# Optimization experiments

Measured on AMD Instinct MI355X. Metric: run time of the kernel, lower is better.

## Reference

```python
import jax, jax.numpy as jnp
import numpy as np

C = 32        # channels
B = 4         # batch
H = W = 256   # spatial
K = 3         # adaptive kernel size
BN_EPS = 1e-5


def conv2d(x, w, b, pad):
    # x: [B,Cin,H,W], w: [Cout,Cin,kh,kw]
    y = jax.lax.conv_general_dilated(
        x, w, window_strides=(1, 1), padding=[(pad, pad), (pad, pad)],
        dimension_numbers=('NCHW', 'OIHW', 'NCHW'))
    return y + b[None, :, None, None]


def bn(x, g, beta, mu, var):
    scale = (g / jnp.sqrt(var + BN_EPS))[None, :, None, None]
    return (x - mu[None, :, None, None]) * scale + beta[None, :, None, None]


def res_block(x, w, b, g, beta, mu, var):
    # w: [2,C,C,3,3]; conv-BN-ReLU-conv-BN, residual add, ReLU
    h = bn(conv2d(x, w[0], b[0], 1), g[0], beta[0], mu[0], var[0])
    h = jax.nn.relu(h)
    h = bn(conv2d(h, w[1], b[1], 1), g[1], beta[1], mu[1], var[1])
    return jax.nn.relu(x + h)


def kernel_pred(frames, core, rate):
    # frames: [B,N,H,W] (color=1 squeezed), core: [B,N,K*K,H,W]
    b, n, h, w = frames.shape
    p = (K // 2) * rate
    fp = jnp.pad(frames, ((0, 0), (0, 0), (p, p), (p, p)))
    # stack K*K shifted copies along new axis 2 (same order as torch loop)
    stack = jnp.stack([fp[:, :, i * rate:i * rate + h, j * rate:j * rate + w]
                       for i in range(K) for j in range(K)], axis=2)
    return jnp.sum(core * stack, axis=2)  # [B,N,H,W]; white_level=1.0


def setup_inputs() -> dict:
    key = jax.random.key(0)
    ks = jax.random.split(key, 16)
    inp = {}
    inp['input'] = jax.random.normal(ks[0], (B, C, H, W), dtype=jnp.float32)
    # 4 residual blocks x 2 convs each
    inp['wconv'] = 0.05 * jax.random.normal(ks[1], (4, 2, C, C, 3, 3), dtype=jnp.float32)
    inp['bconv'] = jnp.zeros((4, 2, C), dtype=jnp.float32)
    inp['bn_gamma'] = jnp.ones((4, 2, C), dtype=jnp.float32) + 0.01 * jax.random.normal(ks[2], (4, 2, C), dtype=jnp.float32)
    inp['bn_beta'] = 0.01 * jax.random.normal(ks[3], (4, 2, C), dtype=jnp.float32)
    inp['bn_mean'] = 0.1 * jax.random.normal(ks[4], (4, 2, C), dtype=jnp.float32)
    inp['bn_var'] = 0.5 + jax.random.uniform(ks[5], (4, 2, C), dtype=jnp.float32)
    inp['tau'] = 0.5 * jnp.ones((1, C, 1, 1), dtype=jnp.float32)
    inp['w_outc'] = 0.05 * jax.random.normal(ks[6], (C * 9, C, 1, 1), dtype=jnp.float32)
    inp['b_outc'] = jnp.zeros((C * 9,), dtype=jnp.float32)
    inp['w_final'] = 0.05 * jax.random.normal(ks[7], (C, C * 4, 3, 3), dtype=jnp.float32)
    inp['b_final'] = jnp.zeros((C,), dtype=jnp.float32)
    return inp


def reference(input, wconv, bconv, bn_gamma, bn_beta, bn_mean, bn_var, tau,
              w_outc, b_outc, w_final, b_final):
    m = input
    for i in range(4):  # fixed small structural loop over residual blocks
        m = res_block(m, wconv[i], bconv[i], bn_gamma[i], bn_beta[i],
                      bn_mean[i], bn_var[i])
    m5 = jax.nn.relu(m - tau)
    core = conv2d(m5, w_outc, b_outc, 0)                    # [B, C*9, H, W]
    core = core.reshape(B, C, K * K, H, W)                  # [B, N, 9, H, W]
    preds = [kernel_pred(input, core, r) for r in (1, 2, 3, 4)]
    pred_cat = jnp.concatenate(preds, axis=1)               # [B, 4C, H, W]
    return conv2d(pred_cat, w_final, b_final, 1)            # [B, C, H, W]
```

## Files before the change

kernel.cpp:

```cpp
#include <hip/hip_runtime.h>

typedef __bf16 bf16;
typedef __attribute__((ext_vector_type(8))) __bf16 bf16x8;
typedef __attribute__((ext_vector_type(4))) float f32x4;

#define HH 256
#define WW 256
#define BB 4
#define NPIX 65536
#define AS 264
#define APX 69696
#define PS 258
#define PPX 66564

#define GLOAD16(SRC, DST) __builtin_amdgcn_global_load_lds( \
    (const __attribute__((address_space(1))) void*)(SRC),   \
    (__attribute__((address_space(3))) void*)(DST), 16, 0, 0)

__device__ inline bf16x8 bzero8() {
    bf16x8 v;
    #pragma unroll
    for (int i = 0; i < 8; ++i) v[i] = (bf16)0.0f;
    return v;
}

__device__ inline int chof(int s) {
    return 4 * (s >> 3) + 16 * ((s >> 2) & 1) + (s & 3);
}

__global__ __launch_bounds__(256) void prep_in(const float* __restrict__ in,
                                               bf16* __restrict__ outP) {
    int p = blockIdx.x * 256 + threadIdx.x;
    int b = p >> 16, rem = p & 65535;
    int y = rem >> 8, x = rem & 255;
    float ch[32];
    #pragma unroll
    for (int c = 0; c < 32; ++c)
        ch[c] = in[(size_t)(b * 32 + c) * NPIX + rem];
    bf16* o = outP + ((size_t)b * APX + (size_t)(y + 4) * AS + x + 4) * 32;
    #pragma unroll
    for (int g = 0; g < 4; ++g) {
        bf16x8 w;
        #pragma unroll
        for (int j = 0; j < 4; ++j) {
            w[j]     = (bf16)ch[4 * g + j];
            w[4 + j] = (bf16)ch[16 + 4 * g + j];
        }
        *reinterpret_cast<bf16x8*>(o + g * 8) = w;
    }
}

__global__ __launch_bounds__(256) void zero_halo(bf16* __restrict__ in0b,
                                                 bf16* __restrict__ actA,
                                                 bf16* __restrict__ actB,
                                                 bf16* __restrict__ pred) {
    int i = blockIdx.x * 256 + threadIdx.x;
    const int NA = 3 * 4 * 4160;
    if (i < NA) {
        int buf = i / (4 * 4160), r = i % (4 * 4160);
        int b = r / 4160, k = r % 4160;
        int y, x;
        if (k < 2112) { int rr = k / 264; y = rr < 4 ? rr : 256 + rr; x = k % 264; }
        else { int j = k - 2112; y = 4 + j / 8; int c8 = j % 8; x = c8 < 4 ? c8 : 256 + c8; }
        bf16* p = (buf == 0 ? in0b : buf == 1 ? actA : actB) +
                  ((size_t)b * APX + (size_t)y * AS + x) * 32;
        #pragma unroll
        for (int cg = 0; cg < 4; ++cg)
            *reinterpret_cast<bf16x8*>(p + cg * 8) = bzero8();
    } else if (i < NA + 4 * 1028) {
        int r = i - NA;
        int b = r / 1028, k = r % 1028;
        int y, x;
        if (k < 516) { int rr = k / 258; y = rr ? 257 : 0; x = k % 258; }
        else { int j = k - 516; y = 1 + j / 2; x = (j & 1) ? 257 : 0; }
        bf16* p = pred + ((size_t)b * PPX + (size_t)y * PS + x) * 128;
        #pragma unroll
        for (int cg = 0; cg < 16; ++cg)
            *reinterpret_cast<bf16x8*>(p + cg * 8) = bzero8();
    }
}

__global__ void fold_w(const float* __restrict__ wconv, const float* __restrict__ bconv,
                       const float* __restrict__ g, const float* __restrict__ beta,
                       const float* __restrict__ mu, const float* __restrict__ var,
                       const float* __restrict__ w_outc, const float* __restrict__ b_outc,
                       const float* __restrict__ w_final, const float* __restrict__ tau,
                       bf16* __restrict__ Wres, float* __restrict__ Bres,
                       bf16* __restrict__ Wcore, bf16* __restrict__ Wfin,
                       float* __restrict__ bCore, float* __restrict__ tauP) {
    int idx = blockIdx.x * 256 + threadIdx.x;
    if (idx < 73728) {
        int l = idx / 9216, r = idx % 9216;
        int tap = r >> 10, co = (r >> 5) & 31, ci = chof(r & 31);
        float s = g[l * 32 + co] * rsqrtf(var[l * 32 + co] + 1e-5f);
        Wres[idx] = (bf16)(wconv[l * 9216 + (co * 32 + ci) * 9 + tap] * s);
    } else if (idx < 73984) {
        int i = idx - 73728;
        float s = g[i] * rsqrtf(var[i] + 1e-5f);
        Bres[i] = (bconv[i] - mu[i]) * s + beta[i];
    } else if (idx < 83200) {
        int r = idx - 73984;
        int tap = r >> 10, nn = (r >> 5) & 31, ci = chof(r & 31);
        Wcore[r] = (bf16)w_outc[(nn * 9 + tap) * 32 + ci];
    } else if (idx < 120064) {
        int r = idx - 83200;
        int chunk = r / 9216, r2 = r % 9216;
        int tap = r2 >> 10, co = (r2 >> 5) & 31, n = chof(r2 & 31);
        Wfin[r] = (bf16)w_final[(size_t)(co * 128 + chunk * 32 + n) * 9 + tap];
    } else if (idx < 120352) {
        int r = idx - 120064;
        int tap = r >> 5, n = r & 31;
        bCore[r] = b_outc[n * 9 + tap];
    } else if (idx < 120384) {
        int s = idx - 120352;
        tauP[s] = tau[chof(s)];
    }
}

__global__ __launch_bounds__(256) void resblock_g(
    const bf16* __restrict__ in, const bf16* __restrict__ W1,
    const bf16* __restrict__ W2, const float* __restrict__ B1,
    const float* __restrict__ B2, bf16* __restrict__ out) {
    extern __shared__ char smem[];
    bf16* xs = (bf16*)smem;
    bf16* hs = (bf16*)(smem + 34816);
    const int x0 = blockIdx.x * 64, y0 = blockIdx.y * 4, b = blockIdx.z;
    const int tid = threadIdx.x;
    const int lane = tid & 63, wv = tid >> 6;
    const int col = lane & 15, g = lane >> 4;
    const bf16* inb = in + (size_t)b * APX * 32;

    for (int gi = wv; gi < 34; gi += 4) {
        int i = gi * 64 + lane;
        int px = i >> 2, s = i & 3;
        int yy = px / 68, xx = px % 68;
        int gsl = s ^ ((px >> 1) & 3);
        const bf16* src = inb + ((size_t)(y0 + yy + 2) * AS + x0 + xx + 2) * 32 + gsl * 8;
        GLOAD16(src, smem + gi * 1024);
    }

    bf16x8 Wf[9][2];
    #pragma unroll
    for (int tap = 0; tap < 9; ++tap) {
        Wf[tap][0] = *reinterpret_cast<const bf16x8*>(W1 + tap * 1024 + col * 32 + g * 8);
        Wf[tap][1] = *reinterpret_cast<const bf16x8*>(W1 + tap * 1024 + (16 + col) * 32 + g * 8);
    }
    f32x4 bb0 = *reinterpret_cast<const f32x4*>(B1 + 4 * g);
    f32x4 bb1 = *reinterpret_cast<const f32x4*>(B1 + 16 + 4 * g);
    __syncthreads();

    for (int u = wv; u < 30; u += 4) {
        int r = u / 5, s = u - 5 * r;
        int off = s * 16; if (off > 50) off = 50;
        const int hy = y0 + r - 1;
        const int hx = x0 + off + col - 1;
        f32x4 c0 = bb0, c1 = bb1;
        #pragma unroll
        for (int tap = 0; tap < 9; ++tap) {
            const int dy = tap / 3, dx = tap % 3;
            const int px = (r + dy) * 68 + off + col + dx;
            bf16x8 Bf = *reinterpret_cast<const bf16x8*>(
                xs + px * 32 + (g ^ ((px >> 1) & 3)) * 8);
            c0 = __builtin_amdgcn_mfma_f32_16x16x32_bf16(Wf[tap][0], Bf, c0, 0, 0, 0);
            c1 = __builtin_amdgcn_mfma_f32_16x16x32_bf16(Wf[tap][1], Bf, c1, 0, 0, 0);
        }
        bf16x8 o;
        #pragma unroll
        for (int j = 0; j < 4; ++j) {
            o[j]     = (bf16)fmaxf(c0[j], 0.0f);
            o[4 + j] = (bf16)fmaxf(c1[j], 0.0f);
        }
        if ((unsigned)hy >= HH || (unsigned)hx >= WW) o = bzero8();
        *reinterpret_cast<bf16x8*>(hs + (r * 66 + off + col) * 40 + g * 8) = o;
    }

    #pragma unroll
    for (int tap = 0; tap < 9; ++tap) {
        Wf[tap][0] = *reinterpret_cast<const bf16x8*>(W2 + tap * 1024 + col * 32 + g * 8);
        Wf[tap][1] = *reinterpret_cast<const bf16x8*>(W2 + tap * 1024 + (16 + col) * 32 + g * 8);
    }
    bb0 = *reinterpret_cast<const f32x4*>(B2 + 4 * g);
    bb1 = *reinterpret_cast<const f32x4*>(B2 + 16 + 4 * g);
    __syncthreads();

    bf16* outb = out + (size_t)b * APX * 32;
    const int y = y0 + wv;
    #pragma unroll
    for (int sg = 0; sg < 4; ++sg) {
        f32x4 c0 = bb0, c1 = bb1;
        #pragma unroll
        for (int tap = 0; tap < 9; ++tap) {
            const int dy = tap / 3, dx = tap % 3;
            bf16x8 Bf = *reinterpret_cast<const bf16x8*>(
                hs + ((wv + dy) * 66 + sg * 16 + col + dx) * 40 + g * 8);
            c0 = __builtin_amdgcn_mfma_f32_16x16x32_bf16(Wf[tap][0], Bf, c0, 0, 0, 0);
            c1 = __builtin_amdgcn_mfma_f32_16x16x32_bf16(Wf[tap][1], Bf, c1, 0, 0, 0);
        }
        const int pxr = (wv + 2) * 68 + sg * 16 + col + 2;
        bf16x8 xr = *reinterpret_cast<const bf16x8*>(
            xs + pxr * 32 + (g ^ ((pxr >> 1) & 3)) * 8);
        bf16x8 o;
        #pragma unroll
        for (int j = 0; j < 4; ++j) {
            o[j]     = (bf16)fmaxf(c0[j] + (float)xr[j], 0.0f);
            o[4 + j] = (bf16)fmaxf(c1[j] + (float)xr[4 + j], 0.0f);
        }
        *reinterpret_cast<bf16x8*>(
            outb + ((size_t)(y + 4) * AS + x0 + sg * 16 + col + 4) * 32 + g * 8) = o;
    }
}

__global__ __launch_bounds__(256) void final_conv_v5(
    const bf16* __restrict__ pred, const bf16* __restrict__ Wfin,
    const float* __restrict__ bfin, float* __restrict__ out) {
    __shared__ bf16 pt[2][12800];
    const int x0 = blockIdx.x * 64, y0 = blockIdx.y * 4, b = blockIdx.z;
    const int tid = threadIdx.x;
    const int lane = tid & 63, wv = tid >> 6;
    const int col = lane & 15, g = lane >> 4;
    const bf16* pb = pred + (size_t)b * PPX * 128;

    auto stage = [&](int c, int bi) {
        for (int gi = wv; gi < 25; gi += 4) {
            int i = gi * 64 + lane;
            int px = i >> 2; if (px > 395) px = 395;
            int s = i & 3;
            int yy = px / 66, xx = px % 66;
            int gsl = s ^ ((px >> 1) & 3);
            const bf16* src = pb + ((size_t)(y0 + yy) * PS + x0 + xx) * 128 + c * 32 + gsl * 8;
            GLOAD16(src, (char*)&pt[bi][0] + gi * 1024);
        }
    };

    f32x4 a0[4], a1[4];
    {
        f32x4 b0 = *reinterpret_cast<const f32x4*>(bfin + 4 * g);
        f32x4 b1 = *reinterpret_cast<const f32x4*>(bfin + 16 + 4 * g);
        #pragma unroll
        for (int i = 0; i < 4; ++i) { a0[i] = b0; a1[i] = b1; }
    }

    stage(0, 0);
    __syncthreads();

    for (int chunk = 0; chunk < 4; ++chunk) {
        const int cur = chunk & 1;
        bf16x8 Wf[9][2];
        #pragma unroll
        for (int tap = 0; tap < 9; ++tap) {
            Wf[tap][0] = *reinterpret_cast<const bf16x8*>(
                Wfin + chunk * 9216 + tap * 1024 + col * 32 + g * 8);
            Wf[tap][1] = *reinterpret_cast<const bf16x8*>(
                Wfin + chunk * 9216 + tap * 1024 + (16 + col) * 32 + g * 8);
        }
        if (chunk < 3) stage(chunk + 1, cur ^ 1);

        #pragma unroll
        for (int sg = 0; sg < 4; ++sg) {
            #pragma unroll
            for (int tap = 0; tap < 9; ++tap) {
                const int dy = tap / 3, dx = tap % 3;
                const int px = (wv + dy) * 66 + sg * 16 + col + dx;
                bf16x8 Bf = *reinterpret_cast<const bf16x8*>(
                    &pt[cur][0] + px * 32 + (g ^ ((px >> 1) & 3)) * 8);
                a0[sg] = __builtin_amdgcn_mfma_f32_16x16x32_bf16(Wf[tap][0], Bf, a0[sg], 0, 0, 0);
                a1[sg] = __builtin_amdgcn_mfma_f32_16x16x32_bf16(Wf[tap][1], Bf, a1[sg], 0, 0, 0);
            }
        }
        __syncthreads();
    }

    const int y = y0 + wv;
    #pragma unroll
    for (int sg = 0; sg < 4; ++sg) {
        const int x = x0 + sg * 16 + col;
        #pragma unroll
        for (int j = 0; j < 4; ++j) {
            out[(size_t)(b * 32 + 4 * g + j) * NPIX + (size_t)y * WW + x] = a0[sg][j];
            out[(size_t)(b * 32 + 16 + 4 * g + j) * NPIX + (size_t)y * WW + x] = a1[sg][j];
        }
    }
}

__global__ __launch_bounds__(256, 2) void core_pred_v4(
    const bf16* __restrict__ m, const bf16* __restrict__ framesP,
    const float* __restrict__ tauP, const bf16* __restrict__ WcoreG,
    const float* __restrict__ bCore, bf16* __restrict__ pred) {
    __shared__ bf16 fr[576 * 32];
    __shared__ bf16 Wc[9 * 32 * 32];
    const int x0 = blockIdx.x * 16, y0 = blockIdx.y * 16, b = blockIdx.z;
    const int tid = threadIdx.x;
    const int lane = tid & 63, wv = tid >> 6;
    const int col = lane & 15, g = lane >> 4;

    for (int i = tid; i < 1152; i += 256)
        *reinterpret_cast<bf16x8*>(Wc + i * 8) =
            *reinterpret_cast<const bf16x8*>(WcoreG + i * 8);
    const bf16* fb = framesP + (size_t)b * APX * 32;
    for (int i = tid; i < 2304; i += 256) {
        int px = i >> 2, cg = i & 3;
        int yy = px / 24, xx = px % 24;
        bf16x8 v = *reinterpret_cast<const bf16x8*>(
            fb + ((size_t)(y0 + yy) * AS + x0 + xx) * 32 + cg * 8);
        *reinterpret_cast<bf16x8*>(fr + px * 32 + cg * 8) = v;
    }
    float t8[8];
    #pragma unroll
    for (int k = 0; k < 8; ++k) t8[k] = tauP[g * 8 + k];
    __syncthreads();

    const bf16* mb = m + (size_t)b * APX * 32;
    bf16* pb = pred + (size_t)b * PPX * 128;

    #pragma unroll 1
    for (int uu = 0; uu < 4; ++uu) {
        const int yl = wv * 4 + uu;
        const int y = y0 + yl;

        bf16x8 Bv = *reinterpret_cast<const bf16x8*>(
            mb + ((size_t)(y + 4) * AS + x0 + col + 4) * 32 + g * 8);
        #pragma unroll
        for (int k = 0; k < 8; ++k)
            Bv[k] = (bf16)fmaxf((float)Bv[k] - t8[k], 0.0f);

        float acc[4][8];
        #pragma unroll
        for (int r = 0; r < 4; ++r)
            #pragma unroll
            for (int k = 0; k < 8; ++k) acc[r][k] = 0.0f;

        #pragma unroll
        for (int dy = 0; dy < 3; ++dy) {
            float core[3][8];
            #pragma unroll
            for (int dx = 0; dx < 3; ++dx) {
                const int tap = dy * 3 + dx;
                bf16x8 A0 = *reinterpret_cast<const bf16x8*>(
                    Wc + tap * 1024 + col * 32 + g * 8);
                bf16x8 A1 = *reinterpret_cast<const bf16x8*>(
                    Wc + tap * 1024 + (16 + col) * 32 + g * 8);
                f32x4 c0 = *reinterpret_cast<const f32x4*>(bCore + tap * 32 + 4 * g);
                f32x4 c1 = *reinterpret_cast<const f32x4*>(bCore + tap * 32 + 16 + 4 * g);
                c0 = __builtin_amdgcn_mfma_f32_16x16x32_bf16(A0, Bv, c0, 0, 0, 0);
                c1 = __builtin_amdgcn_mfma_f32_16x16x32_bf16(A1, Bv, c1, 0, 0, 0);
                #pragma unroll
                for (int j = 0; j < 4; ++j) {
                    core[dx][j]     = c0[j];
                    core[dx][4 + j] = c1[j];
                }
            }
            #pragma unroll
            for (int r = 1; r <= 4; ++r) {
                const int row = yl + 4 + (dy - 1) * r;
                #pragma unroll
                for (int dx = 0; dx < 3; ++dx) {
                    const int cc = col + 4 + (dx - 1) * r;
                    bf16x8 f8 = *reinterpret_cast<const bf16x8*>(
                        fr + (row * 24 + cc) * 32 + g * 8);
                    #pragma unroll
                    for (int k = 0; k < 8; ++k)
                        acc[r - 1][k] += core[dx][k] * (float)f8[k];
                }
            }
        }

        #pragma unroll
        for (int r = 0; r < 4; ++r) {
            bf16x8 o;
            #pragma unroll
            for (int k = 0; k < 8; ++k) o[k] = (bf16)acc[r][k];
            *reinterpret_cast<bf16x8*>(
                pb + ((size_t)(y + 1) * PS + x0 + col + 1) * 128 + r * 32 + g * 8) = o;
        }
    }
}

extern "C" void kernel_launch(void* const* d_in, const int* in_sizes, int n_in,
                              void* d_out, int out_size, void* d_ws, size_t ws_size,
                              hipStream_t stream) {
    const float* input    = (const float*)d_in[0];
    const float* wconv    = (const float*)d_in[1];
    const float* bconv    = (const float*)d_in[2];
    const float* bn_gamma = (const float*)d_in[3];
    const float* bn_beta  = (const float*)d_in[4];
    const float* bn_mean  = (const float*)d_in[5];
    const float* bn_var   = (const float*)d_in[6];
    const float* tau      = (const float*)d_in[7];
    const float* w_outc   = (const float*)d_in[8];
    const float* b_outc   = (const float*)d_in[9];
    const float* w_final  = (const float*)d_in[10];
    const float* b_final  = (const float*)d_in[11];
    float* out = (float*)d_out;

    char* ws = (char*)d_ws;
    bf16*  Wres  = (bf16*)(ws);
    float* Bres  = (float*)(ws + 147456);
    bf16*  Wcore = (bf16*)(ws + 148480);
    bf16*  Wfin  = (bf16*)(ws + 166912);
    float* bCore = (float*)(ws + 240640);
    float* tauP  = (float*)(ws + 241792);
    const size_t ACTB = (size_t)APX * 32 * 2;
    bf16*  in0b  = (bf16*)(ws + 245760);
    bf16*  actA  = (bf16*)(ws + 245760 + 4 * ACTB);
    bf16*  actB  = (bf16*)(ws + 245760 + 8 * ACTB);
    bf16*  pred  = (bf16*)(ws + 245760 + 12 * ACTB);

    hipFuncSetAttribute(reinterpret_cast<const void*>(&resblock_g),
                        hipFuncAttributeMaxDynamicSharedMemorySize, 66560);

    prep_in<<<1024, 256, 0, stream>>>(input, in0b);
    zero_halo<<<212, 256, 0, stream>>>(in0b, actA, actB, pred);
    fold_w<<<471, 256, 0, stream>>>(wconv, bconv, bn_gamma, bn_beta, bn_mean, bn_var,
                                    w_outc, b_outc, w_final, tau,
                                    Wres, Bres, Wcore, Wfin, bCore, tauP);

    dim3 gridr(4, 64, 4), blk(256);
    resblock_g<<<gridr, blk, 66560, stream>>>(in0b, Wres + 0 * 9216, Wres + 1 * 9216,
                                              Bres + 0,  Bres + 32,  actA);
    resblock_g<<<gridr, blk, 66560, stream>>>(actA, Wres + 2 * 9216, Wres + 3 * 9216,
                                              Bres + 64, Bres + 96,  actB);
    resblock_g<<<gridr, blk, 66560, stream>>>(actB, Wres + 4 * 9216, Wres + 5 * 9216,
                                              Bres + 128, Bres + 160, actA);
    resblock_g<<<gridr, blk, 66560, stream>>>(actA, Wres + 6 * 9216, Wres + 7 * 9216,
                                              Bres + 192, Bres + 224, actB);

    dim3 gridp(16, 16, 4);
    core_pred_v4<<<gridp, dim3(256), 0, stream>>>(actB, in0b, tauP, Wcore, bCore, pred);

    dim3 gridf(4, 64, 4);
    final_conv_v5<<<gridf, dim3(256), 0, stream>>>(pred, Wfin, b_final, out);
}
```

Baseline: 186.6 us.

## Enlarge conv tiles to 8 rows and reuse each LDS fragment across output rows

The residual-block and final 3x3 conv kernels now use 512-thread blocks covering 8 output rows instead of 4. Each wave computes a 4-row by 16-column strip and reuses every input fragment it loads from LDS across up to three output rows, which cuts LDS reads per MFMA and shrinks the row halo overhead of the fused two-conv residual block. In exchange, LDS use per block grows substantially and each wave holds 8 accumulator vectors, which may reduce occupancy or raise register pressure.

```diff
diff --git a/kernel.cpp b/kernel.cpp
--- a/kernel.cpp
+++ b/kernel.cpp
@@ -117,20 +117,20 @@
     }
 }
 
-__global__ __launch_bounds__(256) void resblock_g(
+__global__ __launch_bounds__(512) void resblock_v4(
     const bf16* __restrict__ in, const bf16* __restrict__ W1,
     const bf16* __restrict__ W2, const float* __restrict__ B1,
     const float* __restrict__ B2, bf16* __restrict__ out) {
     extern __shared__ char smem[];
     bf16* xs = (bf16*)smem;
-    bf16* hs = (bf16*)(smem + 34816);
-    const int x0 = blockIdx.x * 64, y0 = blockIdx.y * 4, b = blockIdx.z;
+    bf16* hs = (bf16*)(smem + 52224);
+    const int x0 = blockIdx.x * 64, y0 = blockIdx.y * 8, b = blockIdx.z;
     const int tid = threadIdx.x;
     const int lane = tid & 63, wv = tid >> 6;
     const int col = lane & 15, g = lane >> 4;
     const bf16* inb = in + (size_t)b * APX * 32;
 
-    for (int gi = wv; gi < 34; gi += 4) {
+    for (int gi = wv; gi < 51; gi += 8) {
         int i = gi * 64 + lane;
         int px = i >> 2, s = i & 3;
         int yy = px / 68, xx = px % 68;
@@ -149,29 +149,43 @@
     f32x4 bb1 = *reinterpret_cast<const f32x4*>(B1 + 16 + 4 * g);
     __syncthreads();
 
-    for (int u = wv; u < 30; u += 4) {
-        int r = u / 5, s = u - 5 * r;
-        int off = s * 16; if (off > 50) off = 50;
-        const int hy = y0 + r - 1;
-        const int hx = x0 + off + col - 1;
-        f32x4 c0 = bb0, c1 = bb1;
-        #pragma unroll
-        for (int tap = 0; tap < 9; ++tap) {
-            const int dy = tap / 3, dx = tap % 3;
-            const int px = (r + dy) * 68 + off + col + dx;
-            bf16x8 Bf = *reinterpret_cast<const bf16x8*>(
-                xs + px * 32 + (g ^ ((px >> 1) & 3)) * 8);
-            c0 = __builtin_amdgcn_mfma_f32_16x16x32_bf16(Wf[tap][0], Bf, c0, 0, 0, 0);
-            c1 = __builtin_amdgcn_mfma_f32_16x16x32_bf16(Wf[tap][1], Bf, c1, 0, 0, 0);
-        }
-        bf16x8 o;
-        #pragma unroll
-        for (int j = 0; j < 4; ++j) {
-            o[j]     = (bf16)fmaxf(c0[j], 0.0f);
-            o[4 + j] = (bf16)fmaxf(c1[j], 0.0f);
-        }
-        if ((unsigned)hy >= HH || (unsigned)hx >= WW) o = bzero8();
-        *reinterpret_cast<bf16x8*>(hs + (r * 66 + off + col) * 40 + g * 8) = o;
+    for (int id = wv; id < 15; id += 8) {
+        int u = id / 5, s5 = id % 5;
+        int rb = u * 4; if (rb > 6) rb = 6;
+        int off = s5 * 16; if (off > 50) off = 50;
+        f32x4 c[4][2];
+        #pragma unroll
+        for (int rr = 0; rr < 4; ++rr) { c[rr][0] = bb0; c[rr][1] = bb1; }
+        #pragma unroll
+        for (int d = 0; d < 6; ++d) {
+            #pragma unroll
+            for (int dx = 0; dx < 3; ++dx) {
+                const int px = (rb + d) * 68 + off + col + dx;
+                bf16x8 Bf = *reinterpret_cast<const bf16x8*>(
+                    xs + px * 32 + (g ^ ((px >> 1) & 3)) * 8);
+                #pragma unroll
+                for (int rr = 0; rr < 4; ++rr) {
+                    if (rr <= d && d - rr <= 2) {
+                        const int tap = (d - rr) * 3 + dx;
+                        c[rr][0] = __builtin_amdgcn_mfma_f32_16x16x32_bf16(Wf[tap][0], Bf, c[rr][0], 0, 0, 0);
+                        c[rr][1] = __builtin_amdgcn_mfma_f32_16x16x32_bf16(Wf[tap][1], Bf, c[rr][1], 0, 0, 0);
+                    }
+                }
+            }
+        }
+        #pragma unroll
+        for (int rr = 0; rr < 4; ++rr) {
+            bf16x8 o;
+            #pragma unroll
+            for (int j = 0; j < 4; ++j) {
+                o[j]     = (bf16)fmaxf(c[rr][0][j], 0.0f);
+                o[4 + j] = (bf16)fmaxf(c[rr][1][j], 0.0f);
+            }
+            const int hy = y0 + rb + rr - 1;
+            const int hx = x0 + off + col - 1;
+            if ((unsigned)hy >= HH || (unsigned)hx >= WW) o = bzero8();
+            *reinterpret_cast<bf16x8*>(hs + ((rb + rr) * 66 + off + col) * 40 + g * 8) = o;
+        }
     }
 
     #pragma unroll
@@ -183,61 +197,75 @@
     bb1 = *reinterpret_cast<const f32x4*>(B2 + 16 + 4 * g);
     __syncthreads();
 
-    bf16* outb = out + (size_t)b * APX * 32;
-    const int y = y0 + wv;
-    #pragma unroll
-    for (int sg = 0; sg < 4; ++sg) {
-        f32x4 c0 = bb0, c1 = bb1;
-        #pragma unroll
-        for (int tap = 0; tap < 9; ++tap) {
-            const int dy = tap / 3, dx = tap % 3;
-            bf16x8 Bf = *reinterpret_cast<const bf16x8*>(
-                hs + ((wv + dy) * 66 + sg * 16 + col + dx) * 40 + g * 8);
-            c0 = __builtin_amdgcn_mfma_f32_16x16x32_bf16(Wf[tap][0], Bf, c0, 0, 0, 0);
-            c1 = __builtin_amdgcn_mfma_f32_16x16x32_bf16(Wf[tap][1], Bf, c1, 0, 0, 0);
-        }
-        const int pxr = (wv + 2) * 68 + sg * 16 + col + 2;
-        bf16x8 xr = *reinterpret_cast<const bf16x8*>(
-            xs + pxr * 32 + (g ^ ((pxr >> 1) & 3)) * 8);
-        bf16x8 o;
-        #pragma unroll
-        for (int j = 0; j < 4; ++j) {
-            o[j]     = (bf16)fmaxf(c0[j] + (float)xr[j], 0.0f);
-            o[4 + j] = (bf16)fmaxf(c1[j] + (float)xr[4 + j], 0.0f);
-        }
-        *reinterpret_cast<bf16x8*>(
-            outb + ((size_t)(y + 4) * AS + x0 + sg * 16 + col + 4) * 32 + g * 8) = o;
-    }
-}
-
-__global__ __launch_bounds__(256) void final_conv_v5(
+    {
+        const int rb2 = (wv >> 2) * 4, seg = (wv & 3) * 16;
+        f32x4 c[4][2];
+        #pragma unroll
+        for (int rr = 0; rr < 4; ++rr) { c[rr][0] = bb0; c[rr][1] = bb1; }
+        #pragma unroll
+        for (int d = 0; d < 6; ++d) {
+            #pragma unroll
+            for (int dx = 0; dx < 3; ++dx) {
+                bf16x8 Bf = *reinterpret_cast<const bf16x8*>(
+                    hs + ((rb2 + d) * 66 + seg + col + dx) * 40 + g * 8);
+                #pragma unroll
+                for (int rr = 0; rr < 4; ++rr) {
+                    if (rr <= d && d - rr <= 2) {
+                        const int tap = (d - rr) * 3 + dx;
+                        c[rr][0] = __builtin_amdgcn_mfma_f32_16x16x32_bf16(Wf[tap][0], Bf, c[rr][0], 0, 0, 0);
+                        c[rr][1] = __builtin_amdgcn_mfma_f32_16x16x32_bf16(Wf[tap][1], Bf, c[rr][1], 0, 0, 0);
+                    }
+                }
+            }
+        }
+        bf16* outb = out + (size_t)b * APX * 32;
+        #pragma unroll
+        for (int rr = 0; rr < 4; ++rr) {
+            const int y = rb2 + rr;
+            const int pxr = (y + 2) * 68 + seg + col + 2;
+            bf16x8 xr = *reinterpret_cast<const bf16x8*>(
+                xs + pxr * 32 + (g ^ ((pxr >> 1) & 3)) * 8);
+            bf16x8 o;
+            #pragma unroll
+            for (int j = 0; j < 4; ++j) {
+                o[j]     = (bf16)fmaxf(c[rr][0][j] + (float)xr[j], 0.0f);
+                o[4 + j] = (bf16)fmaxf(c[rr][1][j] + (float)xr[4 + j], 0.0f);
+            }
+            *reinterpret_cast<bf16x8*>(
+                outb + ((size_t)(y0 + y + 4) * AS + x0 + seg + col + 4) * 32 + g * 8) = o;
+        }
+    }
+}
+
+__global__ __launch_bounds__(512) void final_conv_v6(
     const bf16* __restrict__ pred, const bf16* __restrict__ Wfin,
     const float* __restrict__ bfin, float* __restrict__ out) {
-    __shared__ bf16 pt[2][12800];
-    const int x0 = blockIdx.x * 64, y0 = blockIdx.y * 4, b = blockIdx.z;
+    extern __shared__ char smem[];
+    const int x0 = blockIdx.x * 64, y0 = blockIdx.y * 8, b = blockIdx.z;
     const int tid = threadIdx.x;
     const int lane = tid & 63, wv = tid >> 6;
     const int col = lane & 15, g = lane >> 4;
     const bf16* pb = pred + (size_t)b * PPX * 128;
 
     auto stage = [&](int c, int bi) {
-        for (int gi = wv; gi < 25; gi += 4) {
+        for (int gi = wv; gi < 42; gi += 8) {
             int i = gi * 64 + lane;
-            int px = i >> 2; if (px > 395) px = 395;
+            int px = i >> 2; if (px > 659) px = 659;
             int s = i & 3;
             int yy = px / 66, xx = px % 66;
             int gsl = s ^ ((px >> 1) & 3);
             const bf16* src = pb + ((size_t)(y0 + yy) * PS + x0 + xx) * 128 + c * 32 + gsl * 8;
-            GLOAD16(src, (char*)&pt[bi][0] + gi * 1024);
+            GLOAD16(src, smem + bi * 43008 + gi * 1024);
         }
     };
 
-    f32x4 a0[4], a1[4];
+    const int rb = (wv >> 2) * 4, seg = (wv & 3) * 16;
+    f32x4 a[4][2];
     {
         f32x4 b0 = *reinterpret_cast<const f32x4*>(bfin + 4 * g);
         f32x4 b1 = *reinterpret_cast<const f32x4*>(bfin + 16 + 4 * g);
         #pragma unroll
-        for (int i = 0; i < 4; ++i) { a0[i] = b0; a1[i] = b1; }
+        for (int rr = 0; rr < 4; ++rr) { a[rr][0] = b0; a[rr][1] = b1; }
     }
 
     stage(0, 0);
@@ -255,29 +283,35 @@
         }
         if (chunk < 3) stage(chunk + 1, cur ^ 1);
 
-        #pragma unroll
-        for (int sg = 0; sg < 4; ++sg) {
-            #pragma unroll
-            for (int tap = 0; tap < 9; ++tap) {
-                const int dy = tap / 3, dx = tap % 3;
-                const int px = (wv + dy) * 66 + sg * 16 + col + dx;
+        const bf16* pt = (const bf16*)(smem + cur * 43008);
+        #pragma unroll
+        for (int d = 0; d < 6; ++d) {
+            #pragma unroll
+            for (int dx = 0; dx < 3; ++dx) {
+                const int px = (rb + d) * 66 + seg + col + dx;
                 bf16x8 Bf = *reinterpret_cast<const bf16x8*>(
-                    &pt[cur][0] + px * 32 + (g ^ ((px >> 1) & 3)) * 8);
-                a0[sg] = __builtin_amdgcn_mfma_f32_16x16x32_bf16(Wf[tap][0], Bf, a0[sg], 0, 0, 0);
-                a1[sg] = __builtin_amdgcn_mfma_f32_16x16x32_bf16(Wf[tap][1], Bf, a1[sg], 0, 0, 0);
+                    pt + px * 32 + (g ^ ((px >> 1) & 3)) * 8);
+                #pragma unroll
+                for (int rr = 0; rr < 4; ++rr) {
+                    if (rr <= d && d - rr <= 2) {
+                        const int tap = (d - rr) * 3 + dx;
+                        a[rr][0] = __builtin_amdgcn_mfma_f32_16x16x32_bf16(Wf[tap][0], Bf, a[rr][0], 0, 0, 0);
+                        a[rr][1] = __builtin_amdgcn_mfma_f32_16x16x32_bf16(Wf[tap][1], Bf, a[rr][1], 0, 0, 0);
+                    }
+                }
             }
         }
         __syncthreads();
     }
 
-    const int y = y0 + wv;
-    #pragma unroll
-    for (int sg = 0; sg < 4; ++sg) {
-        const int x = x0 + sg * 16 + col;
+    #pragma unroll
+    for (int rr = 0; rr < 4; ++rr) {
+        const int y = y0 + rb + rr;
+        const int x = x0 + seg + col;
         #pragma unroll
         for (int j = 0; j < 4; ++j) {
-            out[(size_t)(b * 32 + 4 * g + j) * NPIX + (size_t)y * WW + x] = a0[sg][j];
-            out[(size_t)(b * 32 + 16 + 4 * g + j) * NPIX + (size_t)y * WW + x] = a1[sg][j];
+            out[(size_t)(b * 32 + 4 * g + j) * NPIX + (size_t)y * WW + x] = a[rr][0][j];
+            out[(size_t)(b * 32 + 16 + 4 * g + j) * NPIX + (size_t)y * WW + x] = a[rr][1][j];
         }
     }
 }
@@ -405,8 +439,10 @@
     bf16*  actB  = (bf16*)(ws + 245760 + 8 * ACTB);
     bf16*  pred  = (bf16*)(ws + 245760 + 12 * ACTB);
 
-    hipFuncSetAttribute(reinterpret_cast<const void*>(&resblock_g),
-                        hipFuncAttributeMaxDynamicSharedMemorySize, 66560);
+    hipFuncSetAttribute(reinterpret_cast<const void*>(&resblock_v4),
+                        hipFuncAttributeMaxDynamicSharedMemorySize, 105024);
+    hipFuncSetAttribute(reinterpret_cast<const void*>(&final_conv_v6),
+                        hipFuncAttributeMaxDynamicSharedMemorySize, 86016);
 
     prep_in<<<1024, 256, 0, stream>>>(input, in0b);
     zero_halo<<<212, 256, 0, stream>>>(in0b, actA, actB, pred);
@@ -414,19 +450,19 @@
                                     w_outc, b_outc, w_final, tau,
                                     Wres, Bres, Wcore, Wfin, bCore, tauP);
 
-    dim3 gridr(4, 64, 4), blk(256);
-    resblock_g<<<gridr, blk, 66560, stream>>>(in0b, Wres + 0 * 9216, Wres + 1 * 9216,
-                                              Bres + 0,  Bres + 32,  actA);
-    resblock_g<<<gridr, blk, 66560, stream>>>(actA, Wres + 2 * 9216, Wres + 3 * 9216,
-                                              Bres + 64, Bres + 96,  actB);
-    resblock_g<<<gridr, blk, 66560, stream>>>(actB, Wres + 4 * 9216, Wres + 5 * 9216,
-                                              Bres + 128, Bres + 160, actA);
-    resblock_g<<<gridr, blk, 66560, stream>>>(actA, Wres + 6 * 9216, Wres + 7 * 9216,
-                                              Bres + 192, Bres + 224, actB);
+    dim3 gridr(4, 32, 4), blkr(512);
+    resblock_v4<<<gridr, blkr, 105024, stream>>>(in0b, Wres + 0 * 9216, Wres + 1 * 9216,
+                                                 Bres + 0,  Bres + 32,  actA);
+    resblock_v4<<<gridr, blkr, 105024, stream>>>(actA, Wres + 2 * 9216, Wres + 3 * 9216,
+                                                 Bres + 64, Bres + 96,  actB);
+    resblock_v4<<<gridr, blkr, 105024, stream>>>(actB, Wres + 4 * 9216, Wres + 5 * 9216,
+                                                 Bres + 128, Bres + 160, actA);
+    resblock_v4<<<gridr, blkr, 105024, stream>>>(actA, Wres + 6 * 9216, Wres + 7 * 9216,
+                                                 Bres + 192, Bres + 224, actB);
 
     dim3 gridp(16, 16, 4);
     core_pred_v4<<<gridp, dim3(256), 0, stream>>>(actB, in0b, tauP, Wcore, bCore, pred);
 
-    dim3 gridf(4, 64, 4);
-    final_conv_v5<<<gridf, dim3(256), 0, stream>>>(pred, Wfin, b_final, out);
-}
+    dim3 gridf(4, 32, 4);
+    final_conv_v6<<<gridf, dim3(512), 86016, stream>>>(pred, Wfin, b_final, out);
+}
```

After: 177.1 us. -5.0%, faster.
